# Kernel optimization log

Measured on AMD Instinct MI355X. Metric: run time of the kernel, lower is better.

## Reference

```python
import jax, jax.numpy as jnp
import numpy as np
from jax import lax

TOP_K = 8

B, S, D, N, R = 32, 128, 512, 131072, 16


def setup_inputs() -> dict:
    key = jax.random.key(0)
    ks = jax.random.split(key, 10)
    return {
        "query": jax.random.normal(ks[0], (B, S, D), jnp.float32),
        "base_memory": jax.random.normal(ks[1], (N, D), jnp.float32) * 0.01,
        "lora_A": jax.random.normal(ks[2], (N, R), jnp.float32) * 0.01,
        "lora_B": jax.random.normal(ks[3], (R, D), jnp.float32) * 0.01,
        "gru_w_ih": jax.random.normal(ks[4], (3 * D, D), jnp.float32) * 0.02,
        "gru_w_hh": jax.random.normal(ks[5], (3 * D, D), jnp.float32) * 0.02,
        "gru_b_ih": jax.random.normal(ks[6], (3 * D,), jnp.float32) * 0.02,
        "gru_b_hh": jax.random.normal(ks[7], (3 * D,), jnpp.float32) if False else jax.random.normal(ks[7], (3 * D,), jnp.float32) * 0.02,
        "wg_w": jax.random.normal(ks[8], (1, D), jnp.float32) * 0.02,
        "wg_b": jnp.zeros((1,), jnp.float32),
    }


def gru_cell(x, h, w_ih, w_hh, b_ih, b_hh):
    # torch.nn.GRUCell math; gates ordered [r, z, n]
    gx = x @ w_ih.T + b_ih            # [B, 3D]
    gh = h @ w_hh.T + b_hh            # [B, 3D]
    gx_r, gx_z, gx_n = jnp.split(gx, 3, axis=-1)
    gh_r, gh_z, gh_n = jnp.split(gh, 3, axis=-1)
    r = jax.nn.sigmoid(gx_r + gh_r)
    z = jax.nn.sigmoid(gx_z + gh_z)
    n = jnp.tanh(gx_n + r * gh_n)
    return (1.0 - z) * n + z * h


def reference(query, base_memory, lora_A, lora_B, gru_w_ih, gru_w_hh, gru_b_ih, gru_b_hh, wg_w, wg_b):
    mem = base_memory + lora_A @ lora_B                 # [N, D]
    q = query.mean(axis=1)                              # [B, D]
    scores = q @ mem.T                                  # [B, N]
    top_scores, top_idx = lax.top_k(scores, TOP_K)      # [B, K]
    retrieved = mem[top_idx]                            # [B, K, D] gather

    h0 = jnp.zeros_like(q)
    hidden = gru_cell(retrieved.sum(axis=1), h0, gru_w_ih, gru_w_hh, gru_b_ih, gru_b_hh)

    write_prob = jax.nn.sigmoid(hidden @ wg_w.T + wg_b)  # [B, 1]
    value = q                                            # value[b, 0] in torch == q[b]

    # Sequential over batch (matches torch loop order); within a batch the
    # top-k indices are distinct so a vectorized scatter-set is exact.
    def step(m, inp):
        idx, p, v = inp                                  # [K], scalar, [D]
        rows = (1.0 - p) * m[idx] + p * v
        return m.at[idx].set(rows), None

    new_mem, _ = lax.scan(step, base_memory, (top_idx, write_prob[:, 0], value))
    return retrieved, hidden, new_mem
```

## Files before the change

kernel.cpp:

```cpp
#include <hip/hip_runtime.h>
#include <math.h>

#define NROWS 131072
#define DDIM  512
#define BB    32
#define SS    128
#define KK    8

__global__ __launch_bounds__(256) void k_qmean(const float* __restrict__ query,
                                               float* __restrict__ q) {
  int idx = blockIdx.x * 256 + threadIdx.x;
  int b = idx >> 9, d = idx & 511;
  const float* p = query + (size_t)b * SS * DDIM + d;
  float s = 0.f;
  #pragma unroll 8
  for (int i = 0; i < SS; ++i) s += p[(size_t)i * DDIM];
  q[idx] = s * (1.0f / 128.0f);
}

__global__ __launch_bounds__(256) void k_mem(const float* __restrict__ base,
                                             const float* __restrict__ A,
                                             const float* __restrict__ Bm,
                                             float* __restrict__ newmem) {
  int gt = blockIdx.x * 256 + threadIdx.x;
  int c = gt & 127;
  int stream = gt >> 7;
  int row0 = stream * 64;
  int srow0 = __builtin_amdgcn_readfirstlane(row0);

  float4 Breg[16];
  #pragma unroll
  for (int r = 0; r < 16; ++r)
    Breg[r] = *(const float4*)(Bm + r * DDIM + 4 * c);

  #pragma unroll 4
  for (int i = 0; i < 64; ++i) {
    int n = row0 + i;
    const float* Ar = A + (size_t)(srow0 + i) * 16;
    float4 acc = *(const float4*)(base + (size_t)n * DDIM + 4 * c);
    #pragma unroll
    for (int r = 0; r < 16; ++r) {
      float a = Ar[r];
      acc.x += a * Breg[r].x; acc.y += a * Breg[r].y;
      acc.z += a * Breg[r].z; acc.w += a * Breg[r].w;
    }
    *(float4*)(newmem + (size_t)n * DDIM + 4 * c) = acc;
  }
}

__global__ __launch_bounds__(256) void k_scores(const float* __restrict__ mem,
                                                const float* __restrict__ q,
                                                float* __restrict__ scores) {
  __shared__ float4 sq[4096];
  int t = threadIdx.x;
  const float4* qg = (const float4*)q;
  #pragma unroll
  for (int u = 0; u < 16; ++u) sq[u * 256 + t] = qg[u * 256 + t];
  __syncthreads();

  int r = blockIdx.x * 256 + t;
  float acc[32];
  #pragma unroll
  for (int b = 0; b < 32; ++b) acc[b] = 0.f;
  const float4* mrow = (const float4*)(mem + (size_t)r * DDIM);
  #pragma unroll 2
  for (int d4 = 0; d4 < 128; ++d4) {
    float4 v = mrow[d4];
    #pragma unroll
    for (int b = 0; b < 32; ++b) {
      float4 qv = sq[b * 128 + d4];
      acc[b] += qv.x*v.x + qv.y*v.y + qv.z*v.z + qv.w*v.w;
    }
  }
  #pragma unroll
  for (int b = 0; b < 32; ++b) scores[(size_t)b * NROWS + r] = acc[b];
}

__device__ __forceinline__ void insert8(float (&v)[8], int (&ix)[8], float x, int i) {
  bool better = (x > v[7]) || (x == v[7] && i < ix[7]);
  if (!better) return;
  v[7] = x; ix[7] = i;
  #pragma unroll
  for (int u = 7; u > 0; --u) {
    bool sw = (v[u] > v[u-1]) || (v[u] == v[u-1] && ix[u] < ix[u-1]);
    if (sw) {
      float tv = v[u]; v[u] = v[u-1]; v[u-1] = tv;
      int ti = ix[u]; ix[u] = ix[u-1]; ix[u-1] = ti;
    }
  }
}

__global__ __launch_bounds__(256) void k_topk1(const float* __restrict__ scores,
                                               float* __restrict__ cval,
                                               int* __restrict__ cidx) {
  __shared__ float lval[256][8]; __shared__ int lidx[256][8];
  __shared__ float mval[32][8];  __shared__ int midx[32][8];
  int b = blockIdx.x >> 4, j = blockIdx.x & 15, t = threadIdx.x;
  const float4* s4 = (const float4*)(scores + (size_t)b * NROWS + j * 8192);

  float v[8]; int ix[8];
  #pragma unroll
  for (int e = 0; e < 8; ++e) { v[e] = -1e30f; ix[e] = 0x7fffffff; }
  #pragma unroll
  for (int i = 0; i < 8; ++i) {
    int f4 = i * 256 + t;
    float4 x = s4[f4];
    int n0 = j * 8192 + f4 * 4;
    insert8(v, ix, x.x, n0);
    insert8(v, ix, x.y, n0 + 1);
    insert8(v, ix, x.z, n0 + 2);
    insert8(v, ix, x.w, n0 + 3);
  }
  #pragma unroll
  for (int e = 0; e < 8; ++e) { lval[t][e] = v[e]; lidx[t][e] = ix[e]; }
  __syncthreads();

  if (t < 32) {
    float mv[8]; int mi[8];
    #pragma unroll
    for (int e = 0; e < 8; ++e) { mv[e] = -1e30f; mi[e] = 0x7fffffff; }
    for (int u = 0; u < 8; ++u) {
      int src = t * 8 + u;
      #pragma unroll
      for (int e = 0; e < 8; ++e) insert8(mv, mi, lval[src][e], lidx[src][e]);
    }
    #pragma unroll
    for (int e = 0; e < 8; ++e) { mval[t][e] = mv[e]; midx[t][e] = mi[e]; }
  }
  __syncthreads();

  if (t == 0) {
    float mv[8]; int mi[8];
    #pragma unroll
    for (int e = 0; e < 8; ++e) { mv[e] = -1e30f; mi[e] = 0x7fffffff; }
    for (int u = 0; u < 32; ++u)
      #pragma unroll
      for (int e = 0; e < 8; ++e) insert8(mv, mi, mval[u][e], midx[u][e]);
    #pragma unroll
    for (int e = 0; e < 8; ++e) {
      cval[(b * 16 + j) * 8 + e] = mv[e];
      cidx[(b * 16 + j) * 8 + e] = mi[e];
    }
  }
}

__global__ __launch_bounds__(128) void k_gather(const float* __restrict__ mem,
                                                const float* __restrict__ cval,
                                                const int* __restrict__ cidx,
                                                int* __restrict__ topidx,
                                                float* __restrict__ retrieved,
                                                float* __restrict__ x) {
  __shared__ float scv[128]; __shared__ int sci[128];
  __shared__ int stop[8];
  int b = blockIdx.x, t = threadIdx.x;
  scv[t] = cval[b * 128 + t];
  sci[t] = cidx[b * 128 + t];
  __syncthreads();
  if (t == 0) {
    float mv[8]; int mi[8];
    #pragma unroll
    for (int e = 0; e < 8; ++e) { mv[e] = -1e30f; mi[e] = 0x7fffffff; }
    for (int u = 0; u < 128; ++u) insert8(mv, mi, scv[u], sci[u]);
    #pragma unroll
    for (int e = 0; e < 8; ++e) { stop[e] = mi[e]; topidx[b * 8 + e] = mi[e]; }
  }
  __syncthreads();

  float4 xs = make_float4(0.f, 0.f, 0.f, 0.f);
  #pragma unroll
  for (int k = 0; k < 8; ++k) {
    int row = stop[k];
    float4 vv = *(const float4*)(mem + (size_t)row * DDIM + 4 * t);
    *(float4*)(retrieved + (size_t)(b * 8 + k) * DDIM + 4 * t) = vv;
    xs.x += vv.x; xs.y += vv.y; xs.z += vv.z; xs.w += vv.w;
  }
  *(float4*)(x + (size_t)b * DDIM + 4 * t) = xs;
}

__global__ __launch_bounds__(512) void k_gru(const float* __restrict__ x,
                                             const float* __restrict__ wih,
                                             const float* __restrict__ bih,
                                             const float* __restrict__ bhh,
                                             const float* __restrict__ wgw,
                                             const float* __restrict__ wgb,
                                             float* __restrict__ hidden,
                                             float* __restrict__ pws) {
  __shared__ float sx[512];
  __shared__ float sred[8];
  int b = blockIdx.x, t = threadIdx.x;
  sx[t] = x[b * 512 + t];
  __syncthreads();
  const float* wr = wih + (size_t)t * 512;
  const float* wz = wih + (size_t)(512 + t) * 512;
  const float* wn = wih + (size_t)(1024 + t) * 512;
  float gr = 0.f, gz = 0.f, gn = 0.f;
  #pragma unroll 4
  for (int d4 = 0; d4 < 128; ++d4) {
    float4 xv = *(const float4*)(sx + 4 * d4);
    float4 a = *(const float4*)(wr + 4 * d4);
    float4 c = *(const float4*)(wz + 4 * d4);
    float4 e = *(const float4*)(wn + 4 * d4);
    gr += a.x*xv.x + a.y*xv.y + a.z*xv.z + a.w*xv.w;
    gz += c.x*xv.x + c.y*xv.y + c.z*xv.z + c.w*xv.w;
    gn += e.x*xv.x + e.y*xv.y + e.z*xv.z + e.w*xv.w;
  }
  float r = 1.f / (1.f + expf(-(gr + bih[t]        + bhh[t])));
  float z = 1.f / (1.f + expf(-(gz + bih[512 + t]  + bhh[512 + t])));
  float n = tanhf(gn + bih[1024 + t] + r * bhh[1024 + t]);
  float h = (1.f - z) * n;
  hidden[b * 512 + t] = h;

  float pw = h * wgw[t];
  #pragma unroll
  for (int off = 32; off > 0; off >>= 1) pw += __shfl_down(pw, off, 64);
  if ((t & 63) == 0) sred[t >> 6] = pw;
  __syncthreads();
  if (t == 0) {
    float ssum = 0.f;
    #pragma unroll
    for (int j = 0; j < 8; ++j) ssum += sred[j];
    pws[b] = 1.f / (1.f + expf(-(ssum + wgb[0])));
  }
}

__global__ __launch_bounds__(256) void k_scatter(float* __restrict__ newmem,
                                                 const int* __restrict__ topidx,
                                                 const float* __restrict__ pws,
                                                 const float* __restrict__ q) {
  int t = threadIdx.x;
  int d = blockIdx.x * 64 + (t & 63);
  int k0 = t >> 6;
  for (int b = 0; b < 32; ++b) {
    float p = pws[b];
    float qv = q[b * 512 + d];
    #pragma unroll
    for (int kk = 0; kk < 2; ++kk) {
      int k = k0 + kk * 4;
      int row = topidx[b * 8 + k];
      size_t off = (size_t)row * 512 + d;
      float m = __hip_atomic_load(newmem + off, __ATOMIC_RELAXED,
                                  __HIP_MEMORY_SCOPE_AGENT);
      __hip_atomic_store(newmem + off, (1.f - p) * m + p * qv,
                         __ATOMIC_RELAXED, __HIP_MEMORY_SCOPE_AGENT);
    }
    __syncthreads();
  }
}

extern "C" void kernel_launch(void* const* d_in, const int* in_sizes, int n_in,
                              void* d_out, int out_size, void* d_ws, size_t ws_size,
                              hipStream_t stream) {
  const float* query = (const float*)d_in[0];
  const float* base  = (const float*)d_in[1];
  const float* lA    = (const float*)d_in[2];
  const float* lB    = (const float*)d_in[3];
  const float* wih   = (const float*)d_in[4];
  const float* bih   = (const float*)d_in[6];
  const float* bhh   = (const float*)d_in[7];
  const float* wgw   = (const float*)d_in[8];
  const float* wgb   = (const float*)d_in[9];

  float* out = (float*)d_out;
  float* retrieved = out;
  float* hidden    = out + 131072;
  float* newmem    = out + 147456;

  float* wq  = (float*)d_ws;
  float* wsc = wq + 16384;
  float* wx  = wsc + 4194304;
  float* wp  = wx + 16384;
  int*   wti = (int*)(wp + 32);
  float* wcv = (float*)(wti + 256);
  int*   wci = (int*)(wcv + 4096);

  k_qmean  <<<64,   256, 0, stream>>>(query, wq);
  k_mem    <<<1024, 256, 0, stream>>>(base, lA, lB, newmem);
  k_scores <<<512,  256, 0, stream>>>(newmem, wq, wsc);
  k_topk1  <<<512,  256, 0, stream>>>(wsc, wcv, wci);
  k_gather <<<32,   128, 0, stream>>>(newmem, wcv, wci, wti, retrieved, wx);
  k_gru    <<<32,   512, 0, stream>>>(wx, wih, bih, bhh, wgw, wgb, hidden, wp);
  k_scatter<<<8,    256, 0, stream>>>(newmem, wti, wp, wq);
}
```

Before: 951.5 us.

## Fuse LoRA memory build with score computation and parallelize query mean

Merges the kernel that forms mem = base + A@B with the scores kernel, so each thread builds its memory row in registers, writes it out, and immediately dots it against all 32 queries. This removes the second full read of the 256 MB memory matrix. The query-mean kernel is also split across more blocks, with a shared-memory partial reduction. In exchange, the fused kernel reloads the B matrix from global memory for every row (meant to be cache hits), and each thread's row walk uses strided rather than coalesced loads and stores.

```diff
diff --git a/kernel.cpp b/kernel.cpp
--- a/kernel.cpp
+++ b/kernel.cpp
@@ -9,48 +9,31 @@
 
 __global__ __launch_bounds__(256) void k_qmean(const float* __restrict__ query,
                                                float* __restrict__ q) {
-  int idx = blockIdx.x * 256 + threadIdx.x;
-  int b = idx >> 9, d = idx & 511;
-  const float* p = query + (size_t)b * SS * DDIM + d;
+  __shared__ float part[256];
+  int b  = blockIdx.x >> 3;
+  int dc = blockIdx.x & 7;
+  int t  = threadIdx.x;
+  int lane = t & 63;
+  int p    = t >> 6;
+  const float* src = query + (size_t)b * SS * DDIM + (size_t)(p * 32) * DDIM
+                   + dc * 64 + lane;
   float s = 0.f;
   #pragma unroll 8
-  for (int i = 0; i < SS; ++i) s += p[(size_t)i * DDIM];
-  q[idx] = s * (1.0f / 128.0f);
-}
-
-__global__ __launch_bounds__(256) void k_mem(const float* __restrict__ base,
-                                             const float* __restrict__ A,
-                                             const float* __restrict__ Bm,
-                                             float* __restrict__ newmem) {
-  int gt = blockIdx.x * 256 + threadIdx.x;
-  int c = gt & 127;
-  int stream = gt >> 7;
-  int row0 = stream * 64;
-  int srow0 = __builtin_amdgcn_readfirstlane(row0);
-
-  float4 Breg[16];
-  #pragma unroll
-  for (int r = 0; r < 16; ++r)
-    Breg[r] = *(const float4*)(Bm + r * DDIM + 4 * c);
-
-  #pragma unroll 4
-  for (int i = 0; i < 64; ++i) {
-    int n = row0 + i;
-    const float* Ar = A + (size_t)(srow0 + i) * 16;
-    float4 acc = *(const float4*)(base + (size_t)n * DDIM + 4 * c);
-    #pragma unroll
-    for (int r = 0; r < 16; ++r) {
-      float a = Ar[r];
-      acc.x += a * Breg[r].x; acc.y += a * Breg[r].y;
-      acc.z += a * Breg[r].z; acc.w += a * Breg[r].w;
-    }
-    *(float4*)(newmem + (size_t)n * DDIM + 4 * c) = acc;
-  }
-}
-
-__global__ __launch_bounds__(256) void k_scores(const float* __restrict__ mem,
-                                                const float* __restrict__ q,
-                                                float* __restrict__ scores) {
+  for (int i = 0; i < 32; ++i) s += src[(size_t)i * DDIM];
+  part[t] = s;
+  __syncthreads();
+  if (t < 64) {
+    float tot = part[t] + part[64 + t] + part[128 + t] + part[192 + t];
+    q[b * DDIM + dc * 64 + t] = tot * (1.0f / 128.0f);
+  }
+}
+
+__global__ __launch_bounds__(256) void k_memscores(const float* __restrict__ base,
+                                                   const float* __restrict__ A,
+                                                   const float* __restrict__ Bm,
+                                                   const float* __restrict__ q,
+                                                   float* __restrict__ newmem,
+                                                   float* __restrict__ scores) {
   __shared__ float4 sq[4096];
   int t = threadIdx.x;
   const float4* qg = (const float4*)q;
@@ -59,19 +42,52 @@
   __syncthreads();
 
   int r = blockIdx.x * 256 + t;
+
+  const float* Ar = A + (size_t)r * 16;
+  float av[16];
+  #pragma unroll
+  for (int j = 0; j < 4; ++j) {
+    float4 a = *(const float4*)(Ar + 4 * j);
+    av[4 * j]     = a.x; av[4 * j + 1] = a.y;
+    av[4 * j + 2] = a.z; av[4 * j + 3] = a.w;
+  }
+
   float acc[32];
   #pragma unroll
   for (int b = 0; b < 32; ++b) acc[b] = 0.f;
-  const float4* mrow = (const float4*)(mem + (size_t)r * DDIM);
-  #pragma unroll 2
-  for (int d4 = 0; d4 < 128; ++d4) {
-    float4 v = mrow[d4];
-    #pragma unroll
-    for (int b = 0; b < 32; ++b) {
-      float4 qv = sq[b * 128 + d4];
-      acc[b] += qv.x*v.x + qv.y*v.y + qv.z*v.z + qv.w*v.w;
-    }
-  }
+
+  const float4* brow = (const float4*)(base + (size_t)r * DDIM);
+  float4*       nrow = (float4*)(newmem + (size_t)r * DDIM);
+
+  float4 cur0 = brow[0], cur1 = brow[1], cur2 = brow[2], cur3 = brow[3];
+
+  for (int g = 0; g < 32; ++g) {
+    int nb = (g < 31) ? 4 * (g + 1) : 0;
+    float4 nxt0 = brow[nb];
+    float4 nxt1 = brow[nb + 1];
+    float4 nxt2 = brow[nb + 2];
+    float4 nxt3 = brow[nb + 3];
+
+    #pragma unroll
+    for (int j = 0; j < 4; ++j) {
+      int d4 = 4 * g + j;
+      float4 m = (j == 0) ? cur0 : (j == 1) ? cur1 : (j == 2) ? cur2 : cur3;
+      #pragma unroll
+      for (int rr = 0; rr < 16; ++rr) {
+        float4 bv = *(const float4*)(Bm + rr * DDIM + 4 * d4);
+        m.x += av[rr] * bv.x; m.y += av[rr] * bv.y;
+        m.z += av[rr] * bv.z; m.w += av[rr] * bv.w;
+      }
+      nrow[d4] = m;
+      #pragma unroll
+      for (int b = 0; b < 32; ++b) {
+        float4 qv = sq[b * 128 + d4];
+        acc[b] += qv.x * m.x + qv.y * m.y + qv.z * m.z + qv.w * m.w;
+      }
+    }
+    cur0 = nxt0; cur1 = nxt1; cur2 = nxt2; cur3 = nxt3;
+  }
+
   #pragma unroll
   for (int b = 0; b < 32; ++b) scores[(size_t)b * NROWS + r] = acc[b];
 }
@@ -273,11 +289,10 @@
   float* wcv = (float*)(wti + 256);
   int*   wci = (int*)(wcv + 4096);
 
-  k_qmean  <<<64,   256, 0, stream>>>(query, wq);
-  k_mem    <<<1024, 256, 0, stream>>>(base, lA, lB, newmem);
-  k_scores <<<512,  256, 0, stream>>>(newmem, wq, wsc);
-  k_topk1  <<<512,  256, 0, stream>>>(wsc, wcv, wci);
-  k_gather <<<32,   128, 0, stream>>>(newmem, wcv, wci, wti, retrieved, wx);
-  k_gru    <<<32,   512, 0, stream>>>(wx, wih, bih, bhh, wgw, wgb, hidden, wp);
-  k_scatter<<<8,    256, 0, stream>>>(newmem, wti, wp, wq);
-}
+  k_qmean    <<<256, 256, 0, stream>>>(query, wq);
+  k_memscores<<<512, 256, 0, stream>>>(base, lA, lB, wq, newmem, wsc);
+  k_topk1    <<<512, 256, 0, stream>>>(wsc, wcv, wci);
+  k_gather   <<<32,  128, 0, stream>>>(newmem, wcv, wci, wti, retrieved, wx);
+  k_gru      <<<32,  512, 0, stream>>>(wx, wih, bih, bhh, wgw, wgb, hidden, wp);
+  k_scatter  <<<8,   256, 0, stream>>>(newmem, wti, wp, wq);
+}
```

Result: slower. 1.004 ms (+5.5%).
